# Performance work log

Hardware: AMD Instinct MI355X
Metric: run time of the kernel (lower is better)

The kernel has to match this reference:

```python
import jax, jax.numpy as jnp
import numpy as np

B, LQ, LC, LN, D, H = 4, 1024, 1024, 1024, 1024, 16
HD = D // H
LS_INIT = 1e-4
RES_MAX = 10.0
EPS = 1e-5


def layernorm(x, g, b):
    mu = jnp.mean(x, axis=-1, keepdims=True)
    var = jnp.var(x, axis=-1, keepdims=True)
    return (x - mu) * jax.lax.rsqrt(var + EPS) * g + b


def setup_inputs() -> dict:
    key = jax.random.key(0)
    ks = jax.random.split(key, 12)
    s = 0.02
    return {
        "tight_tokens": jax.random.normal(ks[0], (B, LQ, D), jnp.float32),
        "context_tokens": jax.random.normal(ks[1], (B, LC, D), jnp.float32),
        "neighborhood_tokens": jax.random.normal(ks[2], (B, LN, D), jnp.float32),
        "ln_q_g": jnp.ones((D,), jnp.float32), "ln_q_b": jnp.zeros((D,), jnp.float32),
        "ln_kv_g": jnp.ones((D,), jnp.float32), "ln_kv_b": jnp.zeros((D,), jnp.float32),
        "in_proj_w": jax.random.normal(ks[3], (3 * D, D), jnp.float32) * s,
        "in_proj_b": jnp.zeros((3 * D,), jnp.float32),
        "out_proj_w": jax.random.normal(ks[4], (D, D), jnp.float32) * s,
        "out_proj_b": jnp.zeros((D,), jnp.float32),
        "cross_gamma": jnp.full((D,), LS_INIT, jnp.float32),
        "ln_f_g": jnp.ones((D,), jnp.float32), "ln_f_b": jnp.zeros((D,), jnp.float32),
        "w1": jax.random.normal(ks[5], (4 * D, D), jnp.float32) * s,
        "b1": jnp.zeros((4 * D,), jnp.float32),
        "w2": jax.random.normal(ks[6], (D, 4 * D), jnp.float32) * s,
        "b2": jnp.zeros((D,), jnp.float32),
        "ffn_gamma": jnp.full((D,), LS_INIT, jnp.float32),
    }


def reference(tight_tokens, context_tokens, neighborhood_tokens,
              ln_q_g, ln_q_b, ln_kv_g, ln_kv_b,
              in_proj_w, in_proj_b, out_proj_w, out_proj_b, cross_gamma,
              ln_f_g, ln_f_b, w1, b1, w2, b2, ffn_gamma):
    kv = jnp.concatenate([context_tokens, neighborhood_tokens], axis=1)  # [B, LKV, D]
    q_in = layernorm(tight_tokens, ln_q_g, ln_q_b)
    kv_in = layernorm(kv, ln_kv_g, ln_kv_b)

    wq, wk, wv = jnp.split(in_proj_w, 3, axis=0)
    bq, bk, bv = jnp.split(in_proj_b, 3, axis=0)
    q = (q_in @ wq.T + bq).reshape(B, LQ, H, HD)
    k = (kv_in @ wk.T + bk).reshape(B, -1, H, HD)
    v = (kv_in @ wv.T + bv).reshape(B, -1, H, HD)

    scores = jnp.einsum('bqhd,bkhd->bhqk', q, k) / jnp.sqrt(jnp.float32(HD))
    attn = jax.nn.softmax(scores, axis=-1)  # [B, H, LQ, LKV]
    ctx = jnp.einsum('bhqk,bkhd->bqhd', attn, v).reshape(B, LQ, D)
    attn_out = ctx @ out_proj_w.T + out_proj_b

    cg = jnp.clip(cross_gamma, -RES_MAX, RES_MAX)
    x = tight_tokens + attn_out * cg

    h = layernorm(x, ln_f_g, ln_f_b)
    h = jax.nn.gelu(h @ w1.T + b1, approximate=False) @ w2.T + b2
    fg = jnp.clip(ffn_gamma, -RES_MAX, RES_MAX)
    x = x + h * fg

    return x, attn.mean(axis=1)
```

## Files before the change

kernel.cpp:

```cpp
#include <hip/hip_runtime.h>
#include <math.h>

typedef unsigned short u16;
typedef __attribute__((ext_vector_type(8))) short bf16x8;
typedef __attribute__((ext_vector_type(4))) float f32x4;

#define MFMA16(a,b,c) __builtin_amdgcn_mfma_f32_16x16x32_bf16(a,b,c,0,0,0)

__device__ __forceinline__ u16 f2bf(float f){
  union { float f; unsigned int u; } x; x.f = f;
  unsigned int r = x.u + 0x7fffu + ((x.u >> 16) & 1u);
  return (u16)(r >> 16);
}

__device__ __forceinline__ void gload16(const void* g, void* lds){
  __builtin_amdgcn_global_load_lds(
    (const __attribute__((address_space(1))) unsigned int*)g,
    (__attribute__((address_space(3))) unsigned int*)lds, 16, 0, 0);
}

__global__ __launch_bounds__(256) void cvt_weights(
    const float* __restrict__ wqkv, const float* __restrict__ wo,
    const float* __restrict__ w1, const float* __restrict__ w2,
    u16* __restrict__ o0, u16* __restrict__ o1,
    u16* __restrict__ o2, u16* __restrict__ o3)
{
  int idx = blockIdx.x * 256 + threadIdx.x;
  const float* src; u16* dst;
  if (idx < 786432)                    { src = wqkv; dst = o0; }
  else if ((idx -= 786432) < 262144)   { src = wo;   dst = o1; }
  else if ((idx -= 262144) < 1048576)  { src = w1;   dst = o2; }
  else { idx -= 1048576;                 src = w2;   dst = o3; }
  float4 v = ((const float4*)src)[idx];
  short4 o;
  o.x = (short)f2bf(v.x); o.y = (short)f2bf(v.y);
  o.z = (short)f2bf(v.z); o.w = (short)f2bf(v.w);
  ((short4*)dst)[idx] = o;
}

template<int MODE>
__global__ __launch_bounds__(256) void ln_kernel(
    const float* __restrict__ s0, const float* __restrict__ s1,
    const float* __restrict__ g, const float* __restrict__ be,
    u16* __restrict__ out)
{
  int row = blockIdx.x, t = threadIdx.x;
  const float* src;
  if (MODE == 1) {
    int b = row >> 11, p = row & 2047;
    src = (p < 1024) ? s0 + ((long)(b*1024 + p))*1024
                     : s1 + ((long)(b*1024 + p - 1024))*1024;
  } else {
    src = s0 + (long)row * 1024;
  }
  float4 v = ((const float4*)src)[t];
  float s  = v.x + v.y + v.z + v.w;
  float ss = v.x*v.x + v.y*v.y + v.z*v.z + v.w*v.w;
  #pragma unroll
  for (int m = 1; m < 64; m <<= 1) { s += __shfl_xor(s, m); ss += __shfl_xor(ss, m); }
  __shared__ float red[8];
  int l = t & 63, w = t >> 6;
  if (l == 0) { red[w*2] = s; red[w*2+1] = ss; }
  __syncthreads();
  s  = red[0] + red[2] + red[4] + red[6];
  ss = red[1] + red[3] + red[5] + red[7];
  float mean = s * (1.0f/1024.0f);
  float var  = ss * (1.0f/1024.0f) - mean*mean;
  float rstd = rsqrtf(var + 1e-5f);
  float4 gv = ((const float4*)g)[t];
  float4 bv = ((const float4*)be)[t];
  short4 o;
  o.x = (short)f2bf((v.x-mean)*rstd*gv.x + bv.x);
  o.y = (short)f2bf((v.y-mean)*rstd*gv.y + bv.y);
  o.z = (short)f2bf((v.z-mean)*rstd*gv.z + bv.z);
  o.w = (short)f2bf((v.w-mean)*rstd*gv.w + bv.w);
  *(short4*)(out + (long)row*1024 + t*4) = o;
}

template<int EPI, int BM>
__global__ __launch_bounds__(256,2) void gemm_bt(
    const u16* __restrict__ A, const u16* __restrict__ Bt,
    int M, int N, int K,
    const float* __restrict__ bias,
    const float* __restrict__ gamma,
    const float* __restrict__ resid,
    float* __restrict__ outf,
    u16* __restrict__ outb0, u16* __restrict__ outb1)
{
  constexpr int MI = BM / 32;
  __shared__ __align__(16) u16 at[BM*64];
  __shared__ __align__(16) u16 bt[128*64];
  int nwg = gridDim.x;
  int bidx = (blockIdx.x & 7) * (nwg >> 3) + (blockIdx.x >> 3);
  int nb = N >> 7;
  int tm = bidx / nb, tn = bidx % nb;
  int m0 = tm * BM, n0 = tn << 7;
  int t = threadIdx.x, l = t & 63, w = t >> 6;
  int wr = (w >> 1) * (BM/2), wc = (w & 1) * 64;
  int fr = l & 15, fq = l >> 4;
  f32x4 acc[MI][4] = {};
  int rr = t >> 3;
  int cb = (t & 7) << 4;
  const char* Ab = (const char*)A;
  const char* Bp = (const char*)Bt;
  long ld = (long)K * 2;
  for (int kt = 0; kt < K; kt += 64) {
    #pragma unroll
    for (int c = 0; c < MI; c++) {
      int row = c*32 + rr;
      gload16(Ab + (long)(m0 + row)*ld + (long)kt*2 + (cb ^ ((row & 7) << 4)),
              (char*)at + c*4096 + w*1024);
    }
    #pragma unroll
    for (int c = 0; c < 4; c++) {
      int row = c*32 + rr;
      gload16(Bp + (long)(n0 + row)*ld + (long)kt*2 + (cb ^ ((row & 7) << 4)),
              (char*)bt + c*4096 + w*1024);
    }
    __syncthreads();
    #pragma unroll
    for (int ka = 0; ka < 2; ka++) {
      bf16x8 af[MI], bfv[4];
      #pragma unroll
      for (int i = 0; i < MI; i++) {
        int ra = wr + i*16 + fr;
        af[i] = *(const bf16x8*)((const char*)at + ra*128 + ((ka*64 + fq*16) ^ ((ra & 7) << 4)));
      }
      #pragma unroll
      for (int j = 0; j < 4; j++) {
        int rb = wc + j*16 + fr;
        bfv[j] = *(const bf16x8*)((const char*)bt + rb*128 + ((ka*64 + fq*16) ^ ((rb & 7) << 4)));
      }
      #pragma unroll
      for (int i = 0; i < MI; i++)
        #pragma unroll
        for (int j = 0; j < 4; j++)
          acc[i][j] = MFMA16(af[i], bfv[j], acc[i][j]);
    }
    __syncthreads();
  }
  #pragma unroll
  for (int i = 0; i < MI; i++) {
    #pragma unroll
    for (int j = 0; j < 4; j++) {
      #pragma unroll
      for (int r = 0; r < 4; r++) {
        int row = m0 + wr + i*16 + fq*4 + r;
        int col = n0 + wc + j*16 + fr;
        float v = acc[i][j][r];
        if constexpr (EPI == 0) {
          float qv = (v + bias[col]) * 0.18033688011112042f;
          int b = row >> 10, lq = row & 1023, h = col >> 6, hd = col & 63;
          outb0[(((long)(b*16 + h)) << 16) + (lq << 6) + hd] = f2bf(qv);
        } else if constexpr (EPI == 1) {
          float u = v + bias[col];
          int b = row >> 11, p = row & 2047;
          if (col < 1024) {
            int h = col >> 6, hd = col & 63;
            outb0[(((long)((b*16 + h)*2048 + p)) << 6) + hd] = f2bf(u);
          } else {
            int c2 = col - 1024, h = c2 >> 6, hd = c2 & 63;
            outb1[(((long)((b*16 + h)*64 + hd)) << 11) + p] = f2bf(u);
          }
        } else if constexpr (EPI == 2) {
          float gs = gamma[col]; gs = fminf(fmaxf(gs, -10.f), 10.f);
          long idx = (long)row*1024 + col;
          outf[idx] = resid[idx] + (v + bias[col]) * gs;
        } else if constexpr (EPI == 3) {
          float u = v + bias[col];
          float ge = 0.5f * u * (1.0f + erff(u * 0.70710678118654752f));
          outb0[(long)row*4096 + col] = f2bf(ge);
        } else {
          float gs = gamma[col]; gs = fminf(fmaxf(gs, -10.f), 10.f);
          long idx = (long)row*1024 + col;
          outf[idx] = resid[idx] + (v + bias[col]) * gs;
        }
      }
    }
  }
}

__global__ __launch_bounds__(256, 3) void flash_fwd(
    const u16* __restrict__ q, const u16* __restrict__ k,
    const u16* __restrict__ vt, u16* __restrict__ ctx,
    float* __restrict__ ilout)
{
  __shared__ __align__(16) u16 ks[2*128*64];
  __shared__ __align__(16) char ps[4*4352];
  int nwg = gridDim.x;
  int bid = (blockIdx.x & 7) * (nwg >> 3) + (blockIdx.x >> 3);
  int qt = bid & 15, h = (bid >> 4) & 15, b = bid >> 8;
  int q0 = qt << 6;
  int t = threadIdx.x, l = t & 63, w = t >> 6;
  int fr = l & 15, fq = l >> 4;
  const char* qb = (const char*)(q  + (((long)(b*16 + h)) << 16));
  const char* kb = (const char*)(k  + (((long)(b*16 + h)) << 17));
  const char* vb = (const char*)(vt + (((long)(b*16 + h)) << 17));
  char* psw = ps + w*4352;
  int rr = t >> 3 & 31;
  int srr = t >> 3;
  int scb = (t & 7) << 4;
  (void)rr;

  #pragma unroll
  for (int c = 0; c < 4; c++) {
    int row = c*32 + srr;
    gload16(kb + (long)row*128 + (scb ^ ((row & 7) << 4)), (char*)ks + c*4096 + w*1024);
  }
  {
    int qr = l >> 3;
    #pragma unroll
    for (int c = 0; c < 2; c++) {
      int row = c*8 + qr;
      gload16(qb + (long)(q0 + w*16 + row)*128 + (scb ^ ((row & 7) << 4)), psw + c*1024);
    }
  }
  asm volatile("s_waitcnt vmcnt(0)" ::: "memory");
  bf16x8 qf0 = *(const bf16x8*)(psw + fr*128 + ((fq*16) ^ ((fr & 7) << 4)));
  bf16x8 qf1 = *(const bf16x8*)(psw + fr*128 + ((64 + fq*16) ^ ((fr & 7) << 4)));
  asm volatile("s_waitcnt lgkmcnt(0)" ::: "memory");
  __builtin_amdgcn_s_barrier();
  asm volatile("" ::: "memory");

  f32x4 cacc[4] = {};
  f32x4 lrun = {0.f, 0.f, 0.f, 0.f};
  int cur = 0;
  for (int kt = 0; kt < 2048; kt += 128) {
    int notlast = (kt + 128 < 2048);
    if (notlast) {
      #pragma unroll
      for (int c = 0; c < 4; c++) {
        int row = c*32 + srr;
        gload16(kb + (long)(kt + 128 + row)*128 + (scb ^ ((row & 7) << 4)),
                (char*)ks + (cur^1)*16384 + c*4096 + w*1024);
      }
    }
    __builtin_amdgcn_sched_barrier(0);
    bf16x8 vfA[2][4];
    #pragma unroll
    for (int cfd = 0; cfd < 2; cfd++) {
      const char* vrow = vb + (long)(cfd*16 + fr)*4096 + (long)kt*2;
      #pragma unroll
      for (int ka = 0; ka < 4; ka++)
        vfA[cfd][ka] = *(const bf16x8*)(vrow + ka*64 + fq*16);
    }
    const char* ksb = (const char*)ks + cur*16384;
    f32x4 sf[8];
    __builtin_amdgcn_s_setprio(1);
    #pragma unroll
    for (int cf = 0; cf < 8; cf++) {
      int row = cf*16 + fr;
      bf16x8 kf0 = *(const bf16x8*)(ksb + row*128 + ((fq*16) ^ ((row & 7) << 4)));
      bf16x8 kf1 = *(const bf16x8*)(ksb + row*128 + ((64 + fq*16) ^ ((row & 7) << 4)));
      f32x4 a = {};
      a = MFMA16(qf0, kf0, a);
      sf[cf] = MFMA16(qf1, kf1, a);
    }
    __builtin_amdgcn_s_setprio(0);
    bf16x8 vfB[2][4];
    #pragma unroll
    for (int cfd = 0; cfd < 2; cfd++) {
      const char* vrow = vb + (long)((cfd+2)*16 + fr)*4096 + (long)kt*2;
      #pragma unroll
      for (int ka = 0; ka < 4; ka++)
        vfB[cfd][ka] = *(const bf16x8*)(vrow + ka*64 + fq*16);
    }
    #pragma unroll
    for (int cf = 0; cf < 8; cf++)
      #pragma unroll
      for (int r = 0; r < 4; r++) {
        float pv = exp2f(sf[cf][r]);
        lrun[r] += pv;
        union { float f; unsigned int u; } pu; pu.f = pv;
        *(u16*)(psw + (fq*4 + r)*272 + ((cf*16 + fr) << 1)) = (u16)(pu.u >> 16);
      }
    bf16x8 pa[4];
    #pragma unroll
    for (int ka = 0; ka < 4; ka++)
      pa[ka] = *(const bf16x8*)(psw + fr*272 + ka*64 + fq*16);
    __builtin_amdgcn_s_setprio(1);
    #pragma unroll
    for (int cfd = 0; cfd < 2; cfd++)
      #pragma unroll
      for (int ka = 0; ka < 4; ka++)
        cacc[cfd] = MFMA16(pa[ka], vfA[cfd][ka], cacc[cfd]);
    #pragma unroll
    for (int cfd = 0; cfd < 2; cfd++)
      #pragma unroll
      for (int ka = 0; ka < 4; ka++)
        cacc[cfd+2] = MFMA16(pa[ka], vfB[cfd][ka], cacc[cfd+2]);
    __builtin_amdgcn_s_setprio(0);
    if (notlast) {
      asm volatile("s_waitcnt vmcnt(0)" ::: "memory");
      __builtin_amdgcn_s_barrier();
      asm volatile("" ::: "memory");
    }
    cur ^= 1;
  }
  float il4[4];
  #pragma unroll
  for (int r = 0; r < 4; r++) {
    float s = lrun[r];
    #pragma unroll
    for (int msk = 1; msk < 16; msk <<= 1) s += __shfl_xor(s, msk, 16);
    il4[r] = 1.0f / s;
  }
  #pragma unroll
  for (int cf = 0; cf < 4; cf++)
    #pragma unroll
    for (int r = 0; r < 4; r++) {
      int row = q0 + w*16 + fq*4 + r;
      int col = h*64 + cf*16 + fr;
      ctx[(long)(b*1024 + row)*1024 + col] = f2bf(cacc[cf][r] * il4[r]);
    }
  if (fr == 0) {
    #pragma unroll
    for (int r = 0; r < 4; r++) {
      int row = q0 + w*16 + fq*4 + r;
      long idx = (((long)(b*16 + h)) << 10) + row;
      ilout[idx] = il4[r];
    }
  }
}

__global__ __launch_bounds__(256,2) void attn_mean(
    const u16* __restrict__ q, const u16* __restrict__ k,
    const float* __restrict__ il,
    float* __restrict__ out)
{
  __shared__ __align__(16) u16 qs[2][128*64];
  __shared__ __align__(16) u16 ks[2][128*64];
  __shared__ __align__(16) float ml[2][128];
  int nwg = gridDim.x;
  int bid = (blockIdx.x & 7) * (nwg >> 3) + (blockIdx.x >> 3);
  int kt = bid & 15, qt = (bid >> 4) & 7, b = bid >> 7;
  int q0 = qt << 7, k0 = kt << 7;
  int t = threadIdx.x, l = t & 63, w = t >> 6;
  int wr = (w >> 1) << 6, wc = (w & 1) << 6;
  int fr = l & 15, fq = l >> 4;
  int rr = t >> 3, cbb = (t & 7) << 4;
  const long bh = (long)b * 16;

#define AM_STAGE(hh, s) do {                                                        \
    const char* qb_ = (const char*)(q + ((bh + (hh)) << 16)) + (long)q0*128;        \
    const char* kb_ = (const char*)(k + ((bh + (hh)) << 17)) + (long)k0*128;        \
    _Pragma("unroll")                                                               \
    for (int c = 0; c < 4; c++) {                                                   \
      int row = c*32 + rr;                                                          \
      int sw = cbb ^ ((row & 7) << 4);                                              \
      gload16(qb_ + (long)row*128 + sw, (char*)qs[s] + c*4096 + w*1024);            \
      gload16(kb_ + (long)row*128 + sw, (char*)ks[s] + c*4096 + w*1024);            \
    }                                                                               \
    if (w == 0 && l < 32) {                                                         \
      gload16((const char*)(il + ((bh + (hh)) << 10) + q0) + l*16, (char*)ml[s]);   \
    }                                                                               \
  } while (0)

  AM_STAGE(0, 0);
  asm volatile("s_waitcnt vmcnt(0)" ::: "memory");
  __builtin_amdgcn_s_barrier();
  asm volatile("" ::: "memory");

  f32x4 macc[4][4] = {};
  for (int h = 0; h < 16; h++) {
    int cur = h & 1;
    if (h < 15) AM_STAGE(h + 1, cur ^ 1);
    const char* qsb = (const char*)qs[cur];
    const char* ksb = (const char*)ks[cur];
    const float* mlb = ml[cur];
    f32x4 ir4[4];
    #pragma unroll
    for (int i = 0; i < 4; i++)
      ir4[i] = *(const f32x4*)(mlb + wr + i*16 + fq*4);
    bf16x8 af[4][2], bf[4][2];
    #pragma unroll
    for (int i = 0; i < 4; i++) {
      int ra = wr + i*16 + fr;
      int rb = wc + i*16 + fr;
      af[i][0] = *(const bf16x8*)(qsb + ra*128 + ((fq*16) ^ ((ra & 7) << 4)));
      af[i][1] = *(const bf16x8*)(qsb + ra*128 + ((64 + fq*16) ^ ((ra & 7) << 4)));
      bf[i][0] = *(const bf16x8*)(ksb + rb*128 + ((fq*16) ^ ((rb & 7) << 4)));
      bf[i][1] = *(const bf16x8*)(ksb + rb*128 + ((64 + fq*16) ^ ((rb & 7) << 4)));
    }
    #pragma unroll
    for (int j = 0; j < 4; j++) {
      f32x4 sf[4];
      __builtin_amdgcn_s_setprio(1);
      #pragma unroll
      for (int i = 0; i < 4; i++) {
        f32x4 a = MFMA16(af[i][0], bf[j][0], {});
        sf[i] = MFMA16(af[i][1], bf[j][1], a);
      }
      __builtin_amdgcn_s_setprio(0);
      #pragma unroll
      for (int i = 0; i < 4; i++)
        #pragma unroll
        for (int r = 0; r < 4; r++)
          macc[i][j][r] += exp2f(sf[i][r]) * ir4[i][r];
    }
    asm volatile("s_waitcnt vmcnt(0)" ::: "memory");
    __builtin_amdgcn_s_barrier();
    asm volatile("" ::: "memory");
  }
#undef AM_STAGE
  #pragma unroll
  for (int i = 0; i < 4; i++)
    #pragma unroll
    for (int j = 0; j < 4; j++)
      #pragma unroll
      for (int r = 0; r < 4; r++) {
        int row = q0 + wr + i*16 + fq*4 + r;
        int col = k0 + wc + j*16 + fr;
        out[((long)(b*1024 + row) << 11) + col] = macc[i][j][r] * 0.0625f;
      }
}

extern "C" void kernel_launch(void* const* d_in, const int* in_sizes, int n_in,
                              void* d_out, int out_size, void* d_ws, size_t ws_size,
                              hipStream_t stream)
{
  (void)in_sizes; (void)n_in; (void)out_size; (void)ws_size;
  const float* tight = (const float*)d_in[0];
  const float* ctxt  = (const float*)d_in[1];
  const float* nbh   = (const float*)d_in[2];
  const float* lnqg  = (const float*)d_in[3];
  const float* lnqb  = (const float*)d_in[4];
  const float* lnkg  = (const float*)d_in[5];
  const float* lnkb  = (const float*)d_in[6];
  const float* wqkv  = (const float*)d_in[7];
  const float* bqkv  = (const float*)d_in[8];
  const float* wo    = (const float*)d_in[9];
  const float* bo    = (const float*)d_in[10];
  const float* cg    = (const float*)d_in[11];
  const float* lnfg  = (const float*)d_in[12];
  const float* lnfb  = (const float*)d_in[13];
  const float* w1    = (const float*)d_in[14];
  const float* b1    = (const float*)d_in[15];
  const float* w2    = (const float*)d_in[16];
  const float* b2    = (const float*)d_in[17];
  const float* fg    = (const float*)d_in[18];

  char* p = (char*)d_ws;
  u16* wqkv_bf = (u16*)p; p += 3072L*1024*2;
  u16* wo_bf   = (u16*)p; p += 1024L*1024*2;
  u16* w1_bf   = (u16*)p; p += 4096L*1024*2;
  u16* w2_bf   = (u16*)p; p += 1024L*4096*2;
  u16* qin_bf  = (u16*)p; p += 4096L*1024*2;
  u16* kvin_bf = (u16*)p; p += 8192L*1024*2;
  u16* q_bf    = (u16*)p; p += 4L*16*1024*64*2;
  u16* k_bf    = (u16*)p; p += 4L*16*2048*64*2;
  u16* vt_bf   = (u16*)p; p += 4L*16*64*2048*2;
  u16* ctx_bf  = (u16*)p; p += 4096L*1024*2;
  float* il_f  = (float*)p; p += 4L*16*1024*4;
  float* x_f   = (float*)p; p += 4096L*1024*4;
  u16* hln_bf  = (u16*)p; p += 4096L*1024*2;
  u16* gelu_bf = (u16*)p; p += 4096L*4096*2;

  float* x_out    = (float*)d_out;
  float* mean_out = x_out + 4194304;

  cvt_weights<<<12288, 256, 0, stream>>>(wqkv, wo, w1, w2, wqkv_bf, wo_bf, w1_bf, w2_bf);
  ln_kernel<0><<<4096, 256, 0, stream>>>(tight, nullptr, lnqg, lnqb, qin_bf);
  ln_kernel<1><<<8192, 256, 0, stream>>>(ctxt, nbh, lnkg, lnkb, kvin_bf);
  gemm_bt<0,64><<<512, 256, 0, stream>>>(qin_bf, wqkv_bf, 4096, 1024, 1024,
                                      bqkv, nullptr, nullptr, nullptr, q_bf, nullptr);
  gemm_bt<1,128><<<1024, 256, 0, stream>>>(kvin_bf, wqkv_bf + 1024L*1024, 8192, 2048, 1024,
                                       bqkv + 1024, nullptr, nullptr, nullptr, k_bf, vt_bf);
  flash_fwd<<<1024, 256, 0, stream>>>(q_bf, k_bf, vt_bf, ctx_bf, il_f);
  attn_mean<<<512, 256, 0, stream>>>(q_bf, k_bf, il_f, mean_out);
  gemm_bt<2,64><<<512, 256, 0, stream>>>(ctx_bf, wo_bf, 4096, 1024, 1024,
                                      bo, cg, tight, x_f, nullptr, nullptr);
  ln_kernel<0><<<4096, 256, 0, stream>>>(x_f, nullptr, lnfg, lnfb, hln_bf);
  gemm_bt<3,128><<<1024, 256, 0, stream>>>(hln_bf, w1_bf, 4096, 4096, 1024,
                                       b1, nullptr, nullptr, nullptr, gelu_bf, nullptr);
  gemm_bt<4,64><<<512, 256, 0, stream>>>(gelu_bf, w2_bf, 4096, 1024, 4096,
                                      b2, fg, x_f, x_out, nullptr, nullptr);
}
```

Before: 437.5 us.

## Double-buffer GEMM tiles and restructure flash attention into single-wave blocks

The GEMM kernel now double-buffers its A/B shared-memory tiles and prefetches the next K-slice while computing the current one, so global-load latency overlaps with MFMA work. The flash attention kernel moves from 256-thread blocks that share 128-key tiles to 64-thread single-wave blocks, each handling 16 query rows with 32-key tiles. Since a block is one wave, it relies on s_waitcnt and drops the block barrier. In exchange, the GEMM uses twice the LDS, which may reduce occupancy. The smaller attention tiles mean each wave reloads K and V, raising global traffic, and the per-iteration MFMA work per wave is smaller.

```diff
diff --git a/kernel.cpp b/kernel.cpp
--- a/kernel.cpp
+++ b/kernel.cpp
@@ -88,8 +88,8 @@
     u16* __restrict__ outb0, u16* __restrict__ outb1)
 {
   constexpr int MI = BM / 32;
-  __shared__ __align__(16) u16 at[BM*64];
-  __shared__ __align__(16) u16 bt[128*64];
+  __shared__ __align__(16) u16 at[2][BM*64];
+  __shared__ __align__(16) u16 bt[2][128*64];
   int nwg = gridDim.x;
   int bidx = (blockIdx.x & 7) * (nwg >> 3) + (blockIdx.x >> 3);
   int nb = N >> 7;
@@ -104,32 +104,39 @@
   const char* Ab = (const char*)A;
   const char* Bp = (const char*)Bt;
   long ld = (long)K * 2;
+
+#define G_STAGE(s, kt) do {                                                        \
+    _Pragma("unroll")                                                              \
+    for (int c = 0; c < MI; c++) {                                                 \
+      int row = c*32 + rr;                                                         \
+      gload16(Ab + (long)(m0 + row)*ld + (long)(kt)*2 + (cb ^ ((row & 7) << 4)),   \
+              (char*)at[s] + c*4096 + w*1024);                                     \
+    }                                                                              \
+    _Pragma("unroll")                                                              \
+    for (int c = 0; c < 4; c++) {                                                  \
+      int row = c*32 + rr;                                                         \
+      gload16(Bp + (long)(n0 + row)*ld + (long)(kt)*2 + (cb ^ ((row & 7) << 4)),   \
+              (char*)bt[s] + c*4096 + w*1024);                                     \
+    }                                                                              \
+  } while (0)
+
+  G_STAGE(0, 0);
+  __syncthreads();
+  int cur = 0;
   for (int kt = 0; kt < K; kt += 64) {
-    #pragma unroll
-    for (int c = 0; c < MI; c++) {
-      int row = c*32 + rr;
-      gload16(Ab + (long)(m0 + row)*ld + (long)kt*2 + (cb ^ ((row & 7) << 4)),
-              (char*)at + c*4096 + w*1024);
-    }
-    #pragma unroll
-    for (int c = 0; c < 4; c++) {
-      int row = c*32 + rr;
-      gload16(Bp + (long)(n0 + row)*ld + (long)kt*2 + (cb ^ ((row & 7) << 4)),
-              (char*)bt + c*4096 + w*1024);
-    }
-    __syncthreads();
+    if (kt + 64 < K) G_STAGE(cur ^ 1, kt + 64);
     #pragma unroll
     for (int ka = 0; ka < 2; ka++) {
       bf16x8 af[MI], bfv[4];
       #pragma unroll
       for (int i = 0; i < MI; i++) {
         int ra = wr + i*16 + fr;
-        af[i] = *(const bf16x8*)((const char*)at + ra*128 + ((ka*64 + fq*16) ^ ((ra & 7) << 4)));
+        af[i] = *(const bf16x8*)((const char*)at[cur] + ra*128 + ((ka*64 + fq*16) ^ ((ra & 7) << 4)));
       }
       #pragma unroll
       for (int j = 0; j < 4; j++) {
         int rb = wc + j*16 + fr;
-        bfv[j] = *(const bf16x8*)((const char*)bt + rb*128 + ((ka*64 + fq*16) ^ ((rb & 7) << 4)));
+        bfv[j] = *(const bf16x8*)((const char*)bt[cur] + rb*128 + ((ka*64 + fq*16) ^ ((rb & 7) << 4)));
       }
       #pragma unroll
       for (int i = 0; i < MI; i++)
@@ -138,7 +145,9 @@
           acc[i][j] = MFMA16(af[i], bfv[j], acc[i][j]);
     }
     __syncthreads();
-  }
+    cur ^= 1;
+  }
+#undef G_STAGE
   #pragma unroll
   for (int i = 0; i < MI; i++) {
     #pragma unroll
@@ -180,75 +189,62 @@
   }
 }
 
-__global__ __launch_bounds__(256, 3) void flash_fwd(
+__global__ __launch_bounds__(64, 4) void flash_fwd(
     const u16* __restrict__ q, const u16* __restrict__ k,
     const u16* __restrict__ vt, u16* __restrict__ ctx,
     float* __restrict__ ilout)
 {
-  __shared__ __align__(16) u16 ks[2*128*64];
-  __shared__ __align__(16) char ps[4*4352];
+  __shared__ __align__(16) u16 ks[2][32*64];
+  __shared__ __align__(16) char ps[2304];
   int nwg = gridDim.x;
   int bid = (blockIdx.x & 7) * (nwg >> 3) + (blockIdx.x >> 3);
-  int qt = bid & 15, h = (bid >> 4) & 15, b = bid >> 8;
-  int q0 = qt << 6;
-  int t = threadIdx.x, l = t & 63, w = t >> 6;
+  int qt = bid & 63, h = (bid >> 6) & 15, b = bid >> 10;
+  int q0 = qt << 4;
+  int l = threadIdx.x & 63;
   int fr = l & 15, fq = l >> 4;
   const char* qb = (const char*)(q  + (((long)(b*16 + h)) << 16));
   const char* kb = (const char*)(k  + (((long)(b*16 + h)) << 17));
   const char* vb = (const char*)(vt + (((long)(b*16 + h)) << 17));
-  char* psw = ps + w*4352;
-  int rr = t >> 3 & 31;
-  int srr = t >> 3;
-  int scb = (t & 7) << 4;
-  (void)rr;
+  int sr = l >> 3, sc = (l & 7) << 4;
 
   #pragma unroll
   for (int c = 0; c < 4; c++) {
-    int row = c*32 + srr;
-    gload16(kb + (long)row*128 + (scb ^ ((row & 7) << 4)), (char*)ks + c*4096 + w*1024);
-  }
-  {
-    int qr = l >> 3;
-    #pragma unroll
-    for (int c = 0; c < 2; c++) {
-      int row = c*8 + qr;
-      gload16(qb + (long)(q0 + w*16 + row)*128 + (scb ^ ((row & 7) << 4)), psw + c*1024);
-    }
+    int row = c*8 + sr;
+    gload16(kb + (long)row*128 + (sc ^ ((row & 7) << 4)), (char*)ks[0] + c*1024);
+  }
+  #pragma unroll
+  for (int c = 0; c < 2; c++) {
+    int row = c*8 + sr;
+    gload16(qb + (long)(q0 + row)*128 + (sc ^ ((row & 7) << 4)), ps + c*1024);
   }
   asm volatile("s_waitcnt vmcnt(0)" ::: "memory");
-  bf16x8 qf0 = *(const bf16x8*)(psw + fr*128 + ((fq*16) ^ ((fr & 7) << 4)));
-  bf16x8 qf1 = *(const bf16x8*)(psw + fr*128 + ((64 + fq*16) ^ ((fr & 7) << 4)));
+  bf16x8 qf0 = *(const bf16x8*)(ps + fr*128 + ((fq*16) ^ ((fr & 7) << 4)));
+  bf16x8 qf1 = *(const bf16x8*)(ps + fr*128 + ((64 + fq*16) ^ ((fr & 7) << 4)));
   asm volatile("s_waitcnt lgkmcnt(0)" ::: "memory");
-  __builtin_amdgcn_s_barrier();
-  asm volatile("" ::: "memory");
+  __builtin_amdgcn_sched_barrier(0);
 
   f32x4 cacc[4] = {};
   f32x4 lrun = {0.f, 0.f, 0.f, 0.f};
   int cur = 0;
-  for (int kt = 0; kt < 2048; kt += 128) {
-    int notlast = (kt + 128 < 2048);
-    if (notlast) {
+  for (int kt = 0; kt < 2048; kt += 32) {
+    bf16x8 vf[4];
+    #pragma unroll
+    for (int cfd = 0; cfd < 4; cfd++)
+      vf[cfd] = *(const bf16x8*)(vb + (long)(cfd*16 + fr)*4096 + (long)(kt + fq*8)*2);
+    if (kt + 32 < 2048) {
       #pragma unroll
       for (int c = 0; c < 4; c++) {
-        int row = c*32 + srr;
-        gload16(kb + (long)(kt + 128 + row)*128 + (scb ^ ((row & 7) << 4)),
-                (char*)ks + (cur^1)*16384 + c*4096 + w*1024);
-      }
-    }
+        int row = c*8 + sr;
+        gload16(kb + (long)(kt + 32 + row)*128 + (sc ^ ((row & 7) << 4)),
+                (char*)ks[cur ^ 1] + c*1024);
+      }
+    }
+    asm volatile("s_waitcnt vmcnt(4)" ::: "memory");
     __builtin_amdgcn_sched_barrier(0);
-    bf16x8 vfA[2][4];
-    #pragma unroll
-    for (int cfd = 0; cfd < 2; cfd++) {
-      const char* vrow = vb + (long)(cfd*16 + fr)*4096 + (long)kt*2;
-      #pragma unroll
-      for (int ka = 0; ka < 4; ka++)
-        vfA[cfd][ka] = *(const bf16x8*)(vrow + ka*64 + fq*16);
-    }
-    const char* ksb = (const char*)ks + cur*16384;
-    f32x4 sf[8];
-    __builtin_amdgcn_s_setprio(1);
-    #pragma unroll
-    for (int cf = 0; cf < 8; cf++) {
+    const char* ksb = (const char*)ks[cur];
+    f32x4 sf[2];
+    #pragma unroll
+    for (int cf = 0; cf < 2; cf++) {
       int row = cf*16 + fr;
       bf16x8 kf0 = *(const bf16x8*)(ksb + row*128 + ((fq*16) ^ ((row & 7) << 4)));
       bf16x8 kf1 = *(const bf16x8*)(ksb + row*128 + ((64 + fq*16) ^ ((row & 7) << 4)));
@@ -256,45 +252,19 @@
       a = MFMA16(qf0, kf0, a);
       sf[cf] = MFMA16(qf1, kf1, a);
     }
-    __builtin_amdgcn_s_setprio(0);
-    bf16x8 vfB[2][4];
-    #pragma unroll
-    for (int cfd = 0; cfd < 2; cfd++) {
-      const char* vrow = vb + (long)((cfd+2)*16 + fr)*4096 + (long)kt*2;
-      #pragma unroll
-      for (int ka = 0; ka < 4; ka++)
-        vfB[cfd][ka] = *(const bf16x8*)(vrow + ka*64 + fq*16);
-    }
-    #pragma unroll
-    for (int cf = 0; cf < 8; cf++)
+    #pragma unroll
+    for (int cf = 0; cf < 2; cf++)
       #pragma unroll
       for (int r = 0; r < 4; r++) {
         float pv = exp2f(sf[cf][r]);
         lrun[r] += pv;
         union { float f; unsigned int u; } pu; pu.f = pv;
-        *(u16*)(psw + (fq*4 + r)*272 + ((cf*16 + fr) << 1)) = (u16)(pu.u >> 16);
-      }
-    bf16x8 pa[4];
-    #pragma unroll
-    for (int ka = 0; ka < 4; ka++)
-      pa[ka] = *(const bf16x8*)(psw + fr*272 + ka*64 + fq*16);
-    __builtin_amdgcn_s_setprio(1);
-    #pragma unroll
-    for (int cfd = 0; cfd < 2; cfd++)
-      #pragma unroll
-      for (int ka = 0; ka < 4; ka++)
-        cacc[cfd] = MFMA16(pa[ka], vfA[cfd][ka], cacc[cfd]);
-    #pragma unroll
-    for (int cfd = 0; cfd < 2; cfd++)
-      #pragma unroll
-      for (int ka = 0; ka < 4; ka++)
-        cacc[cfd+2] = MFMA16(pa[ka], vfB[cfd][ka], cacc[cfd+2]);
-    __builtin_amdgcn_s_setprio(0);
-    if (notlast) {
-      asm volatile("s_waitcnt vmcnt(0)" ::: "memory");
-      __builtin_amdgcn_s_barrier();
-      asm volatile("" ::: "memory");
-    }
+        *(u16*)(ps + (fq*4 + r)*80 + ((cf*16 + fr) << 1)) = (u16)(pu.u >> 16);
+      }
+    bf16x8 pa = *(const bf16x8*)(ps + fr*80 + fq*16);
+    #pragma unroll
+    for (int cfd = 0; cfd < 4; cfd++)
+      cacc[cfd] = MFMA16(pa, vf[cfd], cacc[cfd]);
     cur ^= 1;
   }
   float il4[4];
@@ -309,14 +279,14 @@
   for (int cf = 0; cf < 4; cf++)
     #pragma unroll
     for (int r = 0; r < 4; r++) {
-      int row = q0 + w*16 + fq*4 + r;
+      int row = q0 + fq*4 + r;
       int col = h*64 + cf*16 + fr;
       ctx[(long)(b*1024 + row)*1024 + col] = f2bf(cacc[cf][r] * il4[r]);
     }
   if (fr == 0) {
     #pragma unroll
     for (int r = 0; r < 4; r++) {
-      int row = q0 + w*16 + fq*4 + r;
+      int row = q0 + fq*4 + r;
       long idx = (((long)(b*16 + h)) << 10) + row;
       ilout[idx] = il4[r];
     }
@@ -466,7 +436,7 @@
                                       bqkv, nullptr, nullptr, nullptr, q_bf, nullptr);
   gemm_bt<1,128><<<1024, 256, 0, stream>>>(kvin_bf, wqkv_bf + 1024L*1024, 8192, 2048, 1024,
                                        bqkv + 1024, nullptr, nullptr, nullptr, k_bf, vt_bf);
-  flash_fwd<<<1024, 256, 0, stream>>>(q_bf, k_bf, vt_bf, ctx_bf, il_f);
+  flash_fwd<<<4096, 64, 0, stream>>>(q_bf, k_bf, vt_bf, ctx_bf, il_f);
   attn_mean<<<512, 256, 0, stream>>>(q_bf, k_bf, il_f, mean_out);
   gemm_bt<2,64><<<512, 256, 0, stream>>>(ctx_bf, wo_bf, 4096, 1024, 1024,
                                       bo, cg, tight, x_f, nullptr, nullptr);
```

Result: slower. 474.3 us (+8.4%).

## Shrink flash-attention KV tile to 64 and stage V through LDS

Applied to the files above, without the earlier changes.

The flash attention kernel now walks the key/value sequence in 64-row tiles instead of 128. V is staged through shared memory with swizzled async global-to-LDS loads instead of direct per-thread global reads into registers. Smaller tiles and fewer register arrays allow raising the occupancy hint from 3 to 4 workgroups per CU. The cost is twice as many loop iterations and an extra barrier in each one.

```diff
diff --git a/kernel.cpp b/kernel.cpp
--- a/kernel.cpp
+++ b/kernel.cpp
@@ -180,13 +180,14 @@
   }
 }
 
-__global__ __launch_bounds__(256, 3) void flash_fwd(
+__global__ __launch_bounds__(256, 4) void flash_fwd(
     const u16* __restrict__ q, const u16* __restrict__ k,
     const u16* __restrict__ vt, u16* __restrict__ ctx,
     float* __restrict__ ilout)
 {
-  __shared__ __align__(16) u16 ks[2*128*64];
-  __shared__ __align__(16) char ps[4*4352];
+  __shared__ __align__(16) u16 ks[2][64*64];
+  __shared__ __align__(16) u16 vs[64*64];
+  __shared__ __align__(16) char ps[4*2304];
   int nwg = gridDim.x;
   int bid = (blockIdx.x & 7) * (nwg >> 3) + (blockIdx.x >> 3);
   int qt = bid & 15, h = (bid >> 4) & 15, b = bid >> 8;
@@ -196,23 +197,21 @@
   const char* qb = (const char*)(q  + (((long)(b*16 + h)) << 16));
   const char* kb = (const char*)(k  + (((long)(b*16 + h)) << 17));
   const char* vb = (const char*)(vt + (((long)(b*16 + h)) << 17));
-  char* psw = ps + w*4352;
-  int rr = t >> 3 & 31;
-  int srr = t >> 3;
-  int scb = (t & 7) << 4;
-  (void)rr;
-
-  #pragma unroll
-  for (int c = 0; c < 4; c++) {
-    int row = c*32 + srr;
-    gload16(kb + (long)row*128 + (scb ^ ((row & 7) << 4)), (char*)ks + c*4096 + w*1024);
+  char* psw = ps + w*2304;
+  int rr = t >> 3;
+  int sc = (t & 7) << 4;
+
+  #pragma unroll
+  for (int c = 0; c < 2; c++) {
+    int row = c*32 + rr;
+    gload16(kb + (long)row*128 + (sc ^ ((row & 7) << 4)), (char*)ks[0] + c*4096 + w*1024);
   }
   {
     int qr = l >> 3;
     #pragma unroll
     for (int c = 0; c < 2; c++) {
       int row = c*8 + qr;
-      gload16(qb + (long)(q0 + w*16 + row)*128 + (scb ^ ((row & 7) << 4)), psw + c*1024);
+      gload16(qb + (long)(q0 + w*16 + row)*128 + (sc ^ ((row & 7) << 4)), psw + c*1024);
     }
   }
   asm volatile("s_waitcnt vmcnt(0)" ::: "memory");
@@ -225,30 +224,28 @@
   f32x4 cacc[4] = {};
   f32x4 lrun = {0.f, 0.f, 0.f, 0.f};
   int cur = 0;
-  for (int kt = 0; kt < 2048; kt += 128) {
-    int notlast = (kt + 128 < 2048);
+  for (int kt = 0; kt < 2048; kt += 64) {
+    int notlast = (kt + 64 < 2048);
+    #pragma unroll
+    for (int c = 0; c < 2; c++) {
+      int hd = c*32 + rr;
+      gload16(vb + (long)hd*4096 + (long)kt*2 + (sc ^ ((hd & 7) << 4)),
+              (char*)vs + c*4096 + w*1024);
+    }
     if (notlast) {
       #pragma unroll
-      for (int c = 0; c < 4; c++) {
-        int row = c*32 + srr;
-        gload16(kb + (long)(kt + 128 + row)*128 + (scb ^ ((row & 7) << 4)),
-                (char*)ks + (cur^1)*16384 + c*4096 + w*1024);
+      for (int c = 0; c < 2; c++) {
+        int row = c*32 + rr;
+        gload16(kb + (long)(kt + 64 + row)*128 + (sc ^ ((row & 7) << 4)),
+                (char*)ks[cur ^ 1] + c*4096 + w*1024);
       }
     }
     __builtin_amdgcn_sched_barrier(0);
-    bf16x8 vfA[2][4];
-    #pragma unroll
-    for (int cfd = 0; cfd < 2; cfd++) {
-      const char* vrow = vb + (long)(cfd*16 + fr)*4096 + (long)kt*2;
-      #pragma unroll
-      for (int ka = 0; ka < 4; ka++)
-        vfA[cfd][ka] = *(const bf16x8*)(vrow + ka*64 + fq*16);
-    }
-    const char* ksb = (const char*)ks + cur*16384;
-    f32x4 sf[8];
+    const char* ksb = (const char*)ks[cur];
+    f32x4 sf[4];
     __builtin_amdgcn_s_setprio(1);
     #pragma unroll
-    for (int cf = 0; cf < 8; cf++) {
+    for (int cf = 0; cf < 4; cf++) {
       int row = cf*16 + fr;
       bf16x8 kf0 = *(const bf16x8*)(ksb + row*128 + ((fq*16) ^ ((row & 7) << 4)));
       bf16x8 kf1 = *(const bf16x8*)(ksb + row*128 + ((64 + fq*16) ^ ((row & 7) << 4)));
@@ -257,38 +254,30 @@
       sf[cf] = MFMA16(qf1, kf1, a);
     }
     __builtin_amdgcn_s_setprio(0);
-    bf16x8 vfB[2][4];
-    #pragma unroll
-    for (int cfd = 0; cfd < 2; cfd++) {
-      const char* vrow = vb + (long)((cfd+2)*16 + fr)*4096 + (long)kt*2;
-      #pragma unroll
-      for (int ka = 0; ka < 4; ka++)
-        vfB[cfd][ka] = *(const bf16x8*)(vrow + ka*64 + fq*16);
-    }
-    #pragma unroll
-    for (int cf = 0; cf < 8; cf++)
+    #pragma unroll
+    for (int cf = 0; cf < 4; cf++)
       #pragma unroll
       for (int r = 0; r < 4; r++) {
         float pv = exp2f(sf[cf][r]);
         lrun[r] += pv;
         union { float f; unsigned int u; } pu; pu.f = pv;
-        *(u16*)(psw + (fq*4 + r)*272 + ((cf*16 + fr) << 1)) = (u16)(pu.u >> 16);
-      }
-    bf16x8 pa[4];
-    #pragma unroll
-    for (int ka = 0; ka < 4; ka++)
-      pa[ka] = *(const bf16x8*)(psw + fr*272 + ka*64 + fq*16);
+        *(u16*)(psw + (fq*4 + r)*144 + ((cf*16 + fr) << 1)) = (u16)(pu.u >> 16);
+      }
+    if (notlast) { asm volatile("s_waitcnt vmcnt(2)" ::: "memory"); }
+    else         { asm volatile("s_waitcnt vmcnt(0)" ::: "memory"); }
+    __builtin_amdgcn_s_barrier();
+    asm volatile("" ::: "memory");
+    bf16x8 pa0 = *(const bf16x8*)(psw + fr*144 + fq*16);
+    bf16x8 pa1 = *(const bf16x8*)(psw + fr*144 + 64 + fq*16);
     __builtin_amdgcn_s_setprio(1);
     #pragma unroll
-    for (int cfd = 0; cfd < 2; cfd++)
-      #pragma unroll
-      for (int ka = 0; ka < 4; ka++)
-        cacc[cfd] = MFMA16(pa[ka], vfA[cfd][ka], cacc[cfd]);
-    #pragma unroll
-    for (int cfd = 0; cfd < 2; cfd++)
-      #pragma unroll
-      for (int ka = 0; ka < 4; ka++)
-        cacc[cfd+2] = MFMA16(pa[ka], vfB[cfd][ka], cacc[cfd+2]);
+    for (int cfd = 0; cfd < 4; cfd++) {
+      int hd = cfd*16 + fr;
+      bf16x8 vf0 = *(const bf16x8*)((const char*)vs + hd*128 + ((fq*16) ^ ((hd & 7) << 4)));
+      bf16x8 vf1 = *(const bf16x8*)((const char*)vs + hd*128 + ((64 + fq*16) ^ ((hd & 7) << 4)));
+      cacc[cfd] = MFMA16(pa0, vf0, cacc[cfd]);
+      cacc[cfd] = MFMA16(pa1, vf1, cacc[cfd]);
+    }
     __builtin_amdgcn_s_setprio(0);
     if (notlast) {
       asm volatile("s_waitcnt vmcnt(0)" ::: "memory");
```

New measurement: 377.0 us. 1.16x faster.
